# Performance work log

Measured on AMD Instinct MI355X. Metric: run time of the kernel, lower is better.

The kernel has to match this reference:

```python
import jax, jax.numpy as jnp
import numpy as np

N, E, DIN, D, H, L = 4096, 65536, 128, 256, 4, 3
DH = D // H


def _ln(x, g, b, eps=1e-5):
    m = jnp.mean(x, axis=-1, keepdims=True)
    v = jnp.mean((x - m) ** 2, axis=-1, keepdims=True)
    return (x - m) * jax.lax.rsqrt(v + eps) * g + b


def _gcn(x, w, b, row, col, n):
    # PyG GCNConv: add self-loops, symmetric normalization D^-1/2 A D^-1/2, aggregate at col (target)
    ar = jnp.arange(n, dtype=row.dtype)
    r = jnp.concatenate([row, ar])
    c = jnp.concatenate([col, ar])
    deg = jax.ops.segment_sum(jnp.ones(r.shape[0], x.dtype), c, num_segments=n)
    dinv = jnp.where(deg > 0, deg ** -0.5, 0.0)
    norm = dinv[r] * dinv[c]  # (E+N,)
    msg = x @ w.T  # (N, out)
    return jax.ops.segment_sum(norm[:, None] * msg[r], c, num_segments=n) + b


def setup_inputs() -> dict:
    key = jax.random.key(0)
    ks = jax.random.split(key, 12)
    rnd = lambda i, shape: jax.random.normal(ks[i], shape, jnp.float32) * 0.05
    return {
        "node_features": jax.random.normal(ks[0], (N, DIN), jnp.float32),
        "edge_index": jax.random.randint(ks[1], (2, E), 0, N, jnp.int32),
        "gcn1_w": rnd(2, (D, DIN)), "gcn1_b": jnp.zeros((D,), jnp.float32),
        "gcn2_w": rnd(3, (D, D)), "gcn2_b": jnp.zeros((D,), jnp.float32),
        "edge_w": rnd(4, (H, 3)), "edge_b": jnp.zeros((H,), jnp.float32),
        "proj_w": rnd(5, (D, DIN + D)), "proj_b": jnp.zeros((D,), jnp.float32),
        "wqkv": rnd(6, (L, 3 * D, D)), "bqkv": jnp.zeros((L, 3 * D), jnp.float32),
        "wo": rnd(7, (L, D, D)), "bo": jnp.zeros((L, D), jnp.float32),
        "ffn_w1": rnd(8, (L, 4 * D, D)), "ffn_b1": jnp.zeros((L, 4 * D), jnp.float32),
        "ffn_w2": rnd(9, (L, D, 4 * D)), "ffn_b2": jnp.zeros((L, D), jnp.float32),
        "ln1_g": jnp.ones((L, D), jnp.float32), "ln1_b": jnp.zeros((L, D), jnp.float32),
        "ln2_g": jnp.ones((L, D), jnp.float32), "ln2_b": jnp.zeros((L, D), jnp.float32),
        "out_w": rnd(10, (1, D)), "out_b": jnp.zeros((1,), jnp.float32),
    }


def reference(node_features, edge_index, gcn1_w, gcn1_b, gcn2_w, gcn2_b,
              edge_w, edge_b, proj_w, proj_b, wqkv, bqkv, wo, bo,
              ffn_w1, ffn_b1, ffn_w2, ffn_b2, ln1_g, ln1_b, ln2_g, ln2_b,
              out_w, out_b):
    n = node_features.shape[0]
    row, col = edge_index[0], edge_index[1]
    # two-layer GCN
    h = jax.nn.relu(_gcn(node_features, gcn1_w, gcn1_b, row, col, n))
    g = _gcn(h, gcn2_w, gcn2_b, row, col, n)
    x = jnp.concatenate([node_features, g], axis=-1) @ proj_w.T + proj_b  # (N, D)
    # edge-aware attention bias: per-edge linear+sigmoid scattered into dense (H, N, N)
    feat = jnp.stack([row.astype(x.dtype), col.astype(x.dtype),
                      jnp.ones(row.shape[0], x.dtype)], axis=-1)  # (E, 3)
    bpe = jax.nn.sigmoid(feat @ edge_w.T + edge_b)  # (E, H)
    bias = jnp.zeros((H, n, n), x.dtype).at[:, row, col].set(bpe.T)
    scale = 1.0 / np.sqrt(DH)
    for l in range(L):
        qkv = x @ wqkv[l].T + bqkv[l]
        q, k, v = jnp.split(qkv, 3, axis=-1)
        q = q.reshape(n, H, DH); k = k.reshape(n, H, DH); v = v.reshape(n, H, DH)
        s = jnp.einsum('nhd,mhd->hnm', q, k) * scale + bias
        a = jax.nn.softmax(s, axis=-1)
        o = jnp.einsum('hnm,mhd->nhd', a, v).reshape(n, D) @ wo[l].T + bo[l]
        x = _ln(x + o, ln1_g[l], ln1_b[l])
        f = jax.nn.relu(x @ ffn_w1[l].T + ffn_b1[l]) @ ffn_w2[l].T + ffn_b2[l]
        x = _ln(x + f, ln2_g[l], ln2_b[l])
    return jax.nn.sigmoid(x @ out_w.T + out_b)  # (N, 1) probs
```

## Files before the change

kernel.cpp:

```cpp
#include <hip/hip_runtime.h>
#include <math.h>

#define NN 4096
#define NE 65536
#define DIN 128
#define DM 256
#define NH 4
#define NL 3
#define NCH 4
#define TPC (NN / 64 / NCH)
#define NBKT 16384

typedef __attribute__((ext_vector_type(8))) short bf16x8;
typedef __attribute__((ext_vector_type(4))) float f32x4;

__device__ inline ushort f2b(float f) {
    union { float f; uint u; } v; v.f = f;
    uint r = v.u + 0x7fffu + ((v.u >> 16) & 1u);
    return (ushort)(r >> 16);
}

__device__ inline uint cvt_pk_bf16(float lo, float hi) {
    uint r;
    asm("v_cvt_pk_bf16_f32 %0, %1, %2" : "=v"(r) : "v"(lo), "v"(hi));
    return r;
}

__device__ inline void gl_lds16(const ushort* g, ushort* l) {
    __builtin_amdgcn_global_load_lds(
        (const __attribute__((address_space(1))) void*)g,
        (__attribute__((address_space(3))) void*)l, 16, 0, 0);
}


__global__ void k_edge1(const int* __restrict__ row, const int* __restrict__ col,
                        uint* __restrict__ bitmap, int* __restrict__ cnt_c,
                        int* __restrict__ bcnt, unsigned char* __restrict__ flag) {
    int e = blockIdx.x * 256 + threadIdx.x;
    if (e >= NE) return;
    int r = row[e], c = col[e];
    atomicAdd(&cnt_c[c], 1);
    uint idx = (uint)r * 4096u + (uint)c;
    uint m = 1u << (idx & 31);
    uint old = atomicOr(&bitmap[idx >> 5], m);
    int isnew = (old & m) ? 0 : 1;
    flag[e] = (unsigned char)isnew;
    if (isnew) atomicAdd(&bcnt[(r >> 4) * 64 + (c >> 6)], 1);
}

__global__ void k_edge2(const int* __restrict__ row, const int* __restrict__ col,
                        const unsigned char* __restrict__ flag,
                        const int* __restrict__ sc, int* __restrict__ fc, int* __restrict__ csc_row,
                        const int* __restrict__ bstart, int* __restrict__ bfill,
                        uint* __restrict__ entcomb,
                        const float* __restrict__ ew, const float* __restrict__ eb) {
    int e = blockIdx.x * 256 + threadIdx.x;
    if (e >= NE) return;
    int r = row[e], c = col[e];
    csc_row[sc[c] + atomicAdd(&fc[c], 1)] = r;
    if (flag[e]) {
        int key = (r >> 4) * 64 + (c >> 6);
        int pos = bstart[key] + atomicAdd(&bfill[key], 1);
        uint idx = (uint)(((r & 15) << 6) | (c & 63));
        float fr = (float)r, fc2 = (float)c;
#pragma unroll
        for (int h = 0; h < NH; ++h) {
            float arg = ew[h * 3 + 0] * fr + ew[h * 3 + 1] * fc2 + ew[h * 3 + 2] + eb[h];
            float sig = 1.f / (1.f + __expf(-arg));
            entcomb[(long)h * NE + pos] = idx | ((uint)f2b(sig) << 16);
        }
    }
}

template <int N>
__global__ void k_scan(const int* __restrict__ cnt, int* __restrict__ start) {
    __shared__ int part[256];
    const int C = N / 256;
    int t = threadIdx.x;
    int s = 0;
    for (int i = 0; i < C; ++i) s += cnt[t * C + i];
    part[t] = s;
    __syncthreads();
    if (t == 0) {
        int acc = 0;
        for (int i = 0; i < 256; ++i) { int v = part[i]; part[i] = acc; acc += v; }
        start[N] = acc;
    }
    __syncthreads();
    int acc = part[t];
    for (int i = 0; i < C; ++i) { start[t * C + i] = acc; acc += cnt[t * C + i]; }
}

__global__ void k_dinv(const int* __restrict__ cnt_c, float* __restrict__ dinv) {
    int i = blockIdx.x * 256 + threadIdx.x;
    if (i < NN) dinv[i] = 1.0f / sqrtf((float)(cnt_c[i] + 1));
}

struct CvtP { const float* s[8]; ushort* d[8]; int n[8]; };
__global__ void k_cvt(CvtP p) {
    int y = blockIdx.y;
    int base = (blockIdx.x * 256 + threadIdx.x) * 4;
    if (base >= p.n[y]) return;
    float4 v = *(const float4*)(p.s[y] + base);
    float sc = 1.f;
    if (y == 1 && ((base >> 8) % 768) < 256) sc = 0.125f;
    ushort4 o;
    o.x = f2b(v.x * sc); o.y = f2b(v.y * sc); o.z = f2b(v.z * sc); o.w = f2b(v.w * sc);
    *(ushort4*)(p.d[y] + base) = o;
}

__global__ void k_scaleb(const float* __restrict__ b, float* __restrict__ o) {
    int i = blockIdx.x * 256 + threadIdx.x;
    if (i < NL * 768) o[i] = b[i] * (((i % 768) < 256) ? 0.125f : 1.f);
}

template <int FLAGS>
__global__ __launch_bounds__(256) void k_gemm_b(
    const ushort* __restrict__ A, int lda,
    const ushort* __restrict__ B, int ldb,
    float* __restrict__ Cf, ushort* __restrict__ Cb, ushort* __restrict__ Cb2, int ldc,
    int K, const float* __restrict__ bias) {
    __shared__ ushort As[128 * 64];
    __shared__ ushort Bs[128 * 64];
    const int tid = threadIdx.x;
    const int w = tid >> 6, l = tid & 63;
    const int l15 = l & 15, l4 = l >> 4;
    const int row0 = blockIdx.y * 128, col0 = blockIdx.x * 128;
    const int wm = (w >> 1) * 64, wn = (w & 1) * 64;
    f32x4 acc[4][4];
#pragma unroll
    for (int i = 0; i < 4; ++i)
#pragma unroll
        for (int j = 0; j < 4; ++j) acc[i][j] = (f32x4){0.f, 0.f, 0.f, 0.f};
    for (int k0 = 0; k0 < K; k0 += 64) {
#pragma unroll
        for (int i = 0; i < 4; ++i) {
            int ci = tid + 256 * i;
            int r = ci >> 3, s = ci & 7;
            gl_lds16(A + (long)(row0 + r) * lda + k0 + ((s ^ (r & 7)) * 8), &As[ci * 8]);
            gl_lds16(B + (long)(col0 + r) * ldb + k0 + ((s ^ (r & 7)) * 8), &Bs[ci * 8]);
        }
        __syncthreads();
#pragma unroll
        for (int kk = 0; kk < 2; ++kk) {
            bf16x8 af[4], bfr[4];
#pragma unroll
            for (int i = 0; i < 4; ++i) {
                int ar = wm + i * 16 + l15;
                af[i] = *(const bf16x8*)&As[ar * 64 + (((kk * 4 + l4) ^ (ar & 7)) * 8)];
                int br = wn + i * 16 + l15;
                bfr[i] = *(const bf16x8*)&Bs[br * 64 + (((kk * 4 + l4) ^ (br & 7)) * 8)];
            }
#pragma unroll
            for (int i = 0; i < 4; ++i)
#pragma unroll
                for (int j = 0; j < 4; ++j)
                    acc[i][j] = __builtin_amdgcn_mfma_f32_16x16x32_bf16(af[i], bfr[j], acc[i][j], 0, 0, 0);
        }
        __syncthreads();
    }
#pragma unroll
    for (int i = 0; i < 4; ++i)
#pragma unroll
        for (int j = 0; j < 4; ++j) {
            int rb = row0 + wm + i * 16;
            int cb = col0 + wn + j * 16 + l15;
            float bv = bias ? bias[cb] : 0.f;
            if (FLAGS & 16) {
                if (cb < 512) {
#pragma unroll
                    for (int q = 0; q < 4; ++q)
                        Cb[(long)(rb + l4 * 4 + q) * 512 + cb] = f2b(acc[i][j][q] + bv);
                } else {
                    ushort4 o4;
                    o4.x = f2b(acc[i][j][0] + bv);
                    o4.y = f2b(acc[i][j][1] + bv);
                    o4.z = f2b(acc[i][j][2] + bv);
                    o4.w = f2b(acc[i][j][3] + bv);
                    *(ushort4*)(Cb2 + (long)(cb - 512) * NN + rb + l4 * 4) = o4;
                }
            } else if (FLAGS & 8) {
                ushort4 o4;
                o4.x = f2b(acc[i][j][0] + bv);
                o4.y = f2b(acc[i][j][1] + bv);
                o4.z = f2b(acc[i][j][2] + bv);
                o4.w = f2b(acc[i][j][3] + bv);
                *(ushort4*)(Cb + (long)cb * ldc + rb + l4 * 4) = o4;
            } else {
#pragma unroll
                for (int q = 0; q < 4; ++q) {
                    int r = rb + l4 * 4 + q;
                    float v = acc[i][j][q] + bv;
                    if (FLAGS & 4) v = fmaxf(v, 0.f);
                    if (FLAGS & 1) Cf[(long)r * ldc + cb] = v;
                    if (FLAGS & 2) Cb[(long)r * ldc + cb] = f2b(v);
                }
            }
        }
}

__global__ __launch_bounds__(256) void k_gemm_ln(
    const ushort* __restrict__ A, int lda,
    const ushort* __restrict__ B, int ldb, int K,
    const float* __restrict__ bias,
    float* __restrict__ x, ushort* __restrict__ xb,
    const float* __restrict__ gam, const float* __restrict__ bet) {
    __shared__ ushort As[16 * 64];
    __shared__ ushort Bs[256 * 64];
    __shared__ float red[4][16][2];
    const int tid = threadIdx.x;
    const int w = tid >> 6, l = tid & 63;
    const int l15 = l & 15, l4 = l >> 4;
    const int row0 = blockIdx.x * 16;
    f32x4 acc[4];
#pragma unroll
    for (int j = 0; j < 4; ++j) acc[j] = (f32x4){0.f, 0.f, 0.f, 0.f};
    for (int k0 = 0; k0 < K; k0 += 64) {
        if (tid < 128) {
            int r = tid >> 3, s = tid & 7;
            gl_lds16(A + (long)(row0 + r) * lda + k0 + ((s ^ (r & 7)) * 8), &As[tid * 8]);
        }
#pragma unroll
        for (int i = 0; i < 8; ++i) {
            int idx = i * 256 + tid;
            int r = idx >> 3, s = idx & 7;
            gl_lds16(B + (long)r * ldb + k0 + ((s ^ (r & 7)) * 8), &Bs[idx * 8]);
        }
        __syncthreads();
#pragma unroll
        for (int kk = 0; kk < 2; ++kk) {
            bf16x8 af = *(const bf16x8*)&As[l15 * 64 + (((kk * 4 + l4) ^ (l15 & 7)) * 8)];
#pragma unroll
            for (int j = 0; j < 4; ++j) {
                int br = w * 64 + j * 16 + l15;
                bf16x8 bfr = *(const bf16x8*)&Bs[br * 64 + (((kk * 4 + l4) ^ (br & 7)) * 8)];
                acc[j] = __builtin_amdgcn_mfma_f32_16x16x32_bf16(af, bfr, acc[j], 0, 0, 0);
            }
        }
        __syncthreads();
    }
    float val[4][4];
#pragma unroll
    for (int j = 0; j < 4; ++j) {
        int c = w * 64 + j * 16 + l15;
        float bv = bias[c];
#pragma unroll
        for (int q = 0; q < 4; ++q) {
            int r = row0 + l4 * 4 + q;
            val[j][q] = acc[j][q] + bv + x[(long)r * DM + c];
        }
    }
    float sum[4], sq[4];
#pragma unroll
    for (int q = 0; q < 4; ++q) {
        sum[q] = (val[0][q] + val[1][q]) + (val[2][q] + val[3][q]);
        sq[q] = (val[0][q] * val[0][q] + val[1][q] * val[1][q]) +
                (val[2][q] * val[2][q] + val[3][q] * val[3][q]);
    }
#pragma unroll
    for (int o = 1; o < 16; o <<= 1)
#pragma unroll
        for (int q = 0; q < 4; ++q) {
            sum[q] += __shfl_xor(sum[q], o);
            sq[q] += __shfl_xor(sq[q], o);
        }
    if (l15 == 0)
#pragma unroll
        for (int q = 0; q < 4; ++q) {
            red[w][l4 * 4 + q][0] = sum[q];
            red[w][l4 * 4 + q][1] = sq[q];
        }
    __syncthreads();
    float mean[4], rs[4];
#pragma unroll
    for (int q = 0; q < 4; ++q) {
        int rl = l4 * 4 + q;
        float ts = (red[0][rl][0] + red[1][rl][0]) + (red[2][rl][0] + red[3][rl][0]);
        float tq = (red[0][rl][1] + red[1][rl][1]) + (red[2][rl][1] + red[3][rl][1]);
        float m = ts * (1.f / 256.f);
        float var = tq * (1.f / 256.f) - m * m;
        mean[q] = m;
        rs[q] = rsqrtf(var + 1e-5f);
    }
#pragma unroll
    for (int j = 0; j < 4; ++j) {
        int c = w * 64 + j * 16 + l15;
        float gv = gam[c], bv = bet[c];
#pragma unroll
        for (int q = 0; q < 4; ++q) {
            int r = row0 + l4 * 4 + q;
            float ov = (val[j][q] - mean[q]) * rs[q] * gv + bv;
            x[(long)r * DM + c] = ov;
            xb[(long)r * DM + c] = f2b(ov);
        }
    }
}

template <int ACT, int B16>
__global__ void k_gcn_agg(const float* __restrict__ msg, const int* __restrict__ sc,
                          const int* __restrict__ csc_row, const float* __restrict__ dinv,
                          const float* __restrict__ bias,
                          float* __restrict__ outf, ushort* __restrict__ outb) {
    int j = blockIdx.x;
    int d = threadIdx.x;
    float acc = 0.f;
    int a = sc[j], b = sc[j + 1];
    for (int i = a; i < b; ++i) {
        int r = csc_row[i];
        acc += dinv[r] * msg[(long)r * DM + d];
    }
    float dj = dinv[j];
    float v = dj * acc + dj * dj * msg[(long)j * DM + d] + bias[d];
    if (ACT) v = fmaxf(v, 0.f);
    if (B16) outb[(long)j * DM + d] = f2b(v);
    else outf[(long)j * DM + d] = v;
}

__global__ void k_concat(const ushort* __restrict__ nfb, const float* __restrict__ g,
                         ushort* __restrict__ xcb) {
    long i = (long)blockIdx.x * 256 + threadIdx.x;
    if (i >= (long)NN * 384) return;
    int r = (int)(i / 384), c = (int)(i % 384);
    xcb[i] = (c < DIN) ? nfb[(long)r * DIN + c] : f2b(g[(long)r * DM + (c - DIN)]);
}

__global__ __launch_bounds__(256, 4) void k_attn(
    const ushort* __restrict__ qkb, const ushort* __restrict__ vT,
    const int* __restrict__ bstart, const uint* __restrict__ entcomb,
    float* __restrict__ opart, float2* __restrict__ ml) {
    __shared__ ushort Klds[2][4096];
    __shared__ ushort Vlds[2][4096];
    __shared__ ushort Pl[4096];
    const int qb = blockIdx.x, h = blockIdx.y, cz = blockIdx.z;
    const int tid = threadIdx.x, w = tid >> 6, l = tid & 63;
    const int l15 = l & 15, l4 = l >> 4;
    bf16x8 qf[2];
    {
        const ushort* qp = qkb + (long)(qb * 64 + w * 16 + l15) * 512 + h * 64 + l4 * 8;
        qf[0] = *(const bf16x8*)(qp);
        qf[1] = *(const bf16x8*)(qp + 32);
    }
    const ushort* Kb = qkb + 256 + h * 64;
    const ushort* Vb = vT + (long)(h * 64) * NN;
    const uint* ec = entcomb + (long)h * NE;
    f32x4 o[4];
#pragma unroll
    for (int f = 0; f < 4; ++f) o[f] = (f32x4){0.f, 0.f, 0.f, 0.f};
    float m_run = -1e30f, l_run = 0.f;
    char* P = (char*)&Pl[w * 1024];
    const int bktW = (qb * 4 + w) * 64;
    const int t0 = cz * TPC;

    auto stage = [&](int b, int t) {
#pragma unroll
        for (int i = 0; i < 2; ++i) {
            int idx = i * 256 + tid;
            int r = idx >> 3, sl = idx & 7;
            gl_lds16(Kb + (long)(t * 64 + r) * 512 + ((sl ^ (r & 7)) * 8),
                     &Klds[b][idx * 8]);
            gl_lds16(Vb + (long)r * NN + t * 64 + ((sl ^ (r & 7)) * 8),
                     &Vlds[b][idx * 8]);
        }
    };

    int bs_c = bstart[bktW + t0], be_c = bstart[bktW + t0 + 1];
    stage(0, t0);
    int cur = 0;
    for (int tt = 0; tt < TPC; ++tt) {
        const int t = t0 + tt;
        asm volatile("s_waitcnt lgkmcnt(0)" ::: "memory");
        __builtin_amdgcn_s_barrier();
        int bs_n = 0, be_n = 0;
        if (tt + 1 < TPC) {
            stage(cur ^ 1, t + 1);
            bs_n = bstart[bktW + t + 1];
            be_n = bstart[bktW + t + 2];
            asm volatile("s_waitcnt vmcnt(4)" ::: "memory");
        } else {
            asm volatile("s_waitcnt vmcnt(0)" ::: "memory");
        }
        __builtin_amdgcn_sched_barrier(0);
        __builtin_amdgcn_s_barrier();
        __builtin_amdgcn_sched_barrier(0);

        const ushort* Kl = Klds[cur];
        const ushort* Vl = Vlds[cur];
        f32x4 s4[4];
#pragma unroll
        for (int f = 0; f < 4; ++f) {
            int kc = f * 16 + l15;
            bf16x8 k0 = *(const bf16x8*)&Kl[kc * 64 + ((l4 ^ (kc & 7)) * 8)];
            bf16x8 k1 = *(const bf16x8*)&Kl[kc * 64 + (((4 + l4) ^ (kc & 7)) * 8)];
            f32x4 a = (f32x4){0.f, 0.f, 0.f, 0.f};
            a = __builtin_amdgcn_mfma_f32_16x16x32_bf16(k0, qf[0], a, 0, 0, 0);
            a = __builtin_amdgcn_mfma_f32_16x16x32_bf16(k1, qf[1], a, 0, 0, 0);
            s4[f] = a;
        }
        for (int i = bs_c; i < be_c; ++i) {
            uint e = ec[i];
            int r4 = (e >> 6) & 15, c6 = e & 63;
            if (l15 == r4 && ((c6 >> 2) & 3) == l4) {
                union { uint u; float f; } sv;
                sv.u = e & 0xFFFF0000u;
                float sig = sv.f;
                switch (((c6 >> 4) << 2) | (c6 & 3)) {
                    case 0:  s4[0][0] += sig; break; case 1:  s4[0][1] += sig; break;
                    case 2:  s4[0][2] += sig; break; case 3:  s4[0][3] += sig; break;
                    case 4:  s4[1][0] += sig; break; case 5:  s4[1][1] += sig; break;
                    case 6:  s4[1][2] += sig; break; case 7:  s4[1][3] += sig; break;
                    case 8:  s4[2][0] += sig; break; case 9:  s4[2][1] += sig; break;
                    case 10: s4[2][2] += sig; break; case 11: s4[2][3] += sig; break;
                    case 12: s4[3][0] += sig; break; case 13: s4[3][1] += sig; break;
                    case 14: s4[3][2] += sig; break; case 15: s4[3][3] += sig; break;
                }
            }
        }
        float ma = fmaxf(fmaxf(s4[0][0], s4[0][1]), fmaxf(s4[0][2], s4[0][3]));
        float mb = fmaxf(fmaxf(s4[1][0], s4[1][1]), fmaxf(s4[1][2], s4[1][3]));
        float mc = fmaxf(fmaxf(s4[2][0], s4[2][1]), fmaxf(s4[2][2], s4[2][3]));
        float md = fmaxf(fmaxf(s4[3][0], s4[3][1]), fmaxf(s4[3][2], s4[3][3]));
        float me = fmaxf(fmaxf(ma, mb), fmaxf(mc, md));
        me = fmaxf(me, __shfl_xor(me, 16));
        me = fmaxf(me, __shfl_xor(me, 32));
        if (!__all(me <= m_run + 8.f)) {
            float mn = fmaxf(m_run, me);
            float fac = __expf(m_run - mn);
            m_run = mn;
            l_run *= fac;
#pragma unroll
            for (int f = 0; f < 4; ++f)
#pragma unroll
                for (int r = 0; r < 4; ++r) o[f][r] *= fac;
        }
        float rp[4];
#pragma unroll
        for (int f = 0; f < 4; ++f) {
            float p0 = __expf(s4[f][0] - m_run);
            float p1 = __expf(s4[f][1] - m_run);
            float p2 = __expf(s4[f][2] - m_run);
            float p3 = __expf(s4[f][3] - m_run);
            s4[f][0] = p0; s4[f][1] = p1; s4[f][2] = p2; s4[f][3] = p3;
            rp[f] = (p0 + p1) + (p2 + p3);
        }
        float rsum = (rp[0] + rp[1]) + (rp[2] + rp[3]);
        rsum += __shfl_xor(rsum, 16);
        rsum += __shfl_xor(rsum, 32);
        l_run += rsum;
#pragma unroll
        for (int f = 0; f < 4; ++f)
#pragma unroll
            for (int p = 0; p < 2; ++p) {
                uint u = cvt_pk_bf16(s4[f][2 * p], s4[f][2 * p + 1]);
                int slot = f * 2 + (l4 >> 1);
                int byte = l15 * 128 + ((slot ^ (l15 & 7)) << 4) + (l4 & 1) * 8 + p * 4;
                *(uint*)(P + byte) = u;
            }
        asm volatile("s_waitcnt lgkmcnt(0)" ::: "memory");
        __builtin_amdgcn_sched_barrier(0);
#pragma unroll
        for (int ks = 0; ks < 2; ++ks) {
            bf16x8 pb = *(const bf16x8*)(P + l15 * 128 + (((ks * 4 + l4) ^ (l15 & 7)) << 4));
#pragma unroll
            for (int fd = 0; fd < 4; ++fd) {
                int d = fd * 16 + l15;
                bf16x8 vfr = *(const bf16x8*)&Vl[d * 64 + (((ks * 4 + l4) ^ (d & 7)) * 8)];
                o[fd] = __builtin_amdgcn_mfma_f32_16x16x32_bf16(vfr, pb, o[fd], 0, 0, 0);
            }
        }
        bs_c = bs_n; be_c = be_n;
        cur ^= 1;
    }
    long base = (((long)cz * NH + h) * NN + qb * 64 + w * 16 + l15) * 64;
#pragma unroll
    for (int fd = 0; fd < 4; ++fd)
#pragma unroll
        for (int r = 0; r < 4; ++r)
            opart[base + fd * 16 + l4 * 4 + r] = o[fd][r];
    if (l4 == 0)
        ml[((long)cz * NH + h) * NN + qb * 64 + w * 16 + l15] = make_float2(m_run, l_run);
}

__global__ __launch_bounds__(256) void k_comb(const float* __restrict__ opart,
                                              const float2* __restrict__ ml,
                                              ushort* __restrict__ attnOb) {
    int t = blockIdx.x * 256 + threadIdx.x;
    int d = t & 63;
    int r = (t >> 6) & (NN - 1);
    int h = t >> 18;
    float2 mls[NCH];
    float M = -1e30f;
#pragma unroll
    for (int c = 0; c < NCH; ++c) {
        mls[c] = ml[((long)c * NH + h) * NN + r];
        M = fmaxf(M, mls[c].x);
    }
    float s = 0.f, ov = 0.f;
#pragma unroll
    for (int c = 0; c < NCH; ++c) {
        float e = __expf(mls[c].x - M);
        s += mls[c].y * e;
        ov += opart[(((long)c * NH + h) * NN + r) * 64 + d] * e;
    }
    attnOb[(long)r * DM + h * 64 + d] = f2b(ov / s);
}


__global__ void k_out(const float* __restrict__ x, const float* __restrict__ w,
                      const float* __restrict__ b, float* __restrict__ out) {
    int row = blockIdx.x;
    int lane = threadIdx.x;
    float s = 0.f;
#pragma unroll
    for (int i = 0; i < 4; ++i) s += x[(long)row * DM + lane + 64 * i] * w[lane + 64 * i];
#pragma unroll
    for (int o = 1; o < 64; o <<= 1) s += __shfl_xor(s, o);
    if (lane == 0) out[row] = 1.f / (1.f + expf(-(s + b[0])));
}

__global__ void k_sentinel(float* out, int n) {
    int i = blockIdx.x * 256 + threadIdx.x;
    if (i < n) out[i] = 1.0e9f;
}


extern "C" void kernel_launch(void* const* d_in, const int* in_sizes, int n_in,
                              void* d_out, int out_size, void* d_ws, size_t ws_size,
                              hipStream_t stream) {
    const float* nf = (const float*)d_in[0];
    const int* ei = (const int*)d_in[1];
    const int* erow = ei;
    const int* ecol = ei + NE;
    const float* gcn1_w = (const float*)d_in[2];
    const float* gcn1_b = (const float*)d_in[3];
    const float* gcn2_w = (const float*)d_in[4];
    const float* gcn2_b = (const float*)d_in[5];
    const float* edge_w = (const float*)d_in[6];
    const float* edge_b = (const float*)d_in[7];
    const float* proj_w = (const float*)d_in[8];
    const float* proj_b = (const float*)d_in[9];
    const float* wqkv = (const float*)d_in[10];
    const float* bqkv = (const float*)d_in[11];
    const float* wo = (const float*)d_in[12];
    const float* bo = (const float*)d_in[13];
    const float* ffn_w1 = (const float*)d_in[14];
    const float* ffn_b1 = (const float*)d_in[15];
    const float* ffn_w2 = (const float*)d_in[16];
    const float* ffn_b2 = (const float*)d_in[17];
    const float* ln1_g = (const float*)d_in[18];
    const float* ln1_b = (const float*)d_in[19];
    const float* ln2_g = (const float*)d_in[20];
    const float* ln2_b = (const float*)d_in[21];
    const float* out_w = (const float*)d_in[22];
    const float* out_b = (const float*)d_in[23];
    float* out = (float*)d_out;

    char* wp = (char*)d_ws;
    size_t off = 0;
    auto alloc = [&](size_t bytes) -> void* {
        void* p = wp + off;
        off = (off + bytes + 255) & ~(size_t)255;
        return p;
    };
    char* big = (char*)alloc((size_t)NCH * NH * NN * 64 * 4);
    float* msg = (float*)big;
    float* opart = (float*)big;
    ushort* ffnHb = (ushort*)big;
    float* x = (float*)alloc((size_t)NN * DM * 4);
    ushort* xb = (ushort*)alloc((size_t)NN * DM * 2);
    ushort* xcb = (ushort*)alloc((size_t)NN * 384 * 2);
    ushort* hb = (ushort*)alloc((size_t)NN * DM * 2);
    float* g = (float*)alloc((size_t)NN * DM * 4);
    ushort* qkb = (ushort*)alloc((size_t)NN * 512 * 2);
    ushort* vT = (ushort*)alloc((size_t)DM * NN * 2);
    ushort* attnOb = (ushort*)alloc((size_t)NN * DM * 2);
    float2* ml = (float2*)alloc((size_t)NCH * NH * NN * 8);
    ushort* nfb = (ushort*)alloc((size_t)NN * DIN * 2);
    ushort* wqkvb = (ushort*)alloc((size_t)NL * 768 * DM * 2);
    ushort* wob = (ushort*)alloc((size_t)NL * DM * DM * 2);
    ushort* f1b = (ushort*)alloc((size_t)NL * 1024 * DM * 2);
    ushort* f2bw = (ushort*)alloc((size_t)NL * DM * 1024 * 2);
    ushort* g1b = (ushort*)alloc((size_t)DM * DIN * 2);
    ushort* g2b = (ushort*)alloc((size_t)DM * DM * 2);
    ushort* pjb = (ushort*)alloc((size_t)DM * 384 * 2);
    float* bq2 = (float*)alloc((size_t)NL * 768 * 4);
    uint* bitmap = (uint*)alloc((size_t)NN * NN / 8);
    unsigned char* flag = (unsigned char*)alloc(NE);
    int* cnt_c = (int*)alloc((size_t)NN * 4);
    int* bcnt = (int*)alloc((size_t)NBKT * 4);
    int* sc = (int*)alloc((size_t)(NN + 1) * 4);
    int* bstart = (int*)alloc((size_t)(NBKT + 1) * 4);
    int* fc = (int*)alloc((size_t)NN * 4);
    int* bfill = (int*)alloc((size_t)NBKT * 4);
    int* csc_row = (int*)alloc((size_t)NE * 4);
    uint* entcomb = (uint*)alloc((size_t)NH * NE * 4);
    float* dinv = (float*)alloc((size_t)NN * 4);

    if (off > ws_size) {
        k_sentinel<<<(out_size + 255) / 256, 256, 0, stream>>>(out, out_size);
        return;
    }

    hipMemsetAsync(bitmap, 0, (size_t)NN * NN / 8, stream);
    hipMemsetAsync(cnt_c, 0, NN * 4, stream);
    hipMemsetAsync(bcnt, 0, NBKT * 4, stream);
    hipMemsetAsync(fc, 0, NN * 4, stream);
    hipMemsetAsync(bfill, 0, NBKT * 4, stream);
    k_edge1<<<NE / 256, 256, 0, stream>>>(erow, ecol, bitmap, cnt_c, bcnt, flag);
    k_scan<NN><<<1, 256, 0, stream>>>(cnt_c, sc);
    k_scan<NBKT><<<1, 256, 0, stream>>>(bcnt, bstart);
    k_edge2<<<NE / 256, 256, 0, stream>>>(erow, ecol, flag, sc, fc, csc_row, bstart, bfill,
                                          entcomb, edge_w, edge_b);
    k_dinv<<<NN / 256, 256, 0, stream>>>(cnt_c, dinv);

    CvtP cp;
    cp.s[0] = nf;      cp.d[0] = nfb;   cp.n[0] = NN * DIN;
    cp.s[1] = wqkv;    cp.d[1] = wqkvb; cp.n[1] = NL * 768 * DM;
    cp.s[2] = wo;      cp.d[2] = wob;   cp.n[2] = NL * DM * DM;
    cp.s[3] = ffn_w1;  cp.d[3] = f1b;   cp.n[3] = NL * 1024 * DM;
    cp.s[4] = ffn_w2;  cp.d[4] = f2bw;  cp.n[4] = NL * DM * 1024;
    cp.s[5] = gcn1_w;  cp.d[5] = g1b;   cp.n[5] = DM * DIN;
    cp.s[6] = gcn2_w;  cp.d[6] = g2b;   cp.n[6] = DM * DM;
    cp.s[7] = proj_w;  cp.d[7] = pjb;   cp.n[7] = DM * 384;
    k_cvt<<<dim3(768, 8), 256, 0, stream>>>(cp);
    k_scaleb<<<(NL * 768 + 255) / 256, 256, 0, stream>>>(bqkv, bq2);

    k_gemm_b<1><<<dim3(DM / 128, NN / 128), 256, 0, stream>>>(
        nfb, DIN, g1b, DIN, msg, nullptr, nullptr, DM, DIN, nullptr);
    k_gcn_agg<1, 1><<<NN, DM, 0, stream>>>(msg, sc, csc_row, dinv, gcn1_b, nullptr, hb);
    k_gemm_b<1><<<dim3(DM / 128, NN / 128), 256, 0, stream>>>(
        hb, DM, g2b, DM, msg, nullptr, nullptr, DM, DM, nullptr);
    k_gcn_agg<0, 0><<<NN, DM, 0, stream>>>(msg, sc, csc_row, dinv, gcn2_b, g, nullptr);
    k_concat<<<(NN * 384 + 255) / 256, 256, 0, stream>>>(nfb, g, xcb);
    k_gemm_b<3><<<dim3(DM / 128, NN / 128), 256, 0, stream>>>(
        xcb, 384, pjb, 384, x, xb, nullptr, DM, 384, proj_b);

    for (int l = 0; l < NL; ++l) {
        k_gemm_b<18><<<dim3(768 / 128, NN / 128), 256, 0, stream>>>(
            xb, DM, wqkvb + (long)l * 768 * DM, DM, nullptr, qkb, vT, 512, DM,
            bq2 + (long)l * 768);
        k_attn<<<dim3(NN / 64, NH, NCH), 256, 0, stream>>>(
            qkb, vT, bstart, entcomb, opart, ml);
        k_comb<<<NN * NH * 64 / 256, 256, 0, stream>>>(opart, ml, attnOb);
        k_gemm_ln<<<NN / 16, 256, 0, stream>>>(
            attnOb, DM, wob + (long)l * DM * DM, DM, DM, bo + (long)l * DM,
            x, xb, ln1_g + (long)l * DM, ln1_b + (long)l * DM);
        k_gemm_b<6><<<dim3(1024 / 128, NN / 128), 256, 0, stream>>>(
            xb, DM, f1b + (long)l * 1024 * DM, DM, nullptr, ffnHb, nullptr, 1024, DM,
            ffn_b1 + (long)l * 1024);
        k_gemm_ln<<<NN / 16, 256, 0, stream>>>(
            ffnHb, 1024, f2bw + (long)l * DM * 1024, 1024, 1024, ffn_b2 + (long)l * DM,
            x, xb, ln2_g + (long)l * DM, ln2_b + (long)l * DM);
    }
    k_out<<<NN, 64, 0, stream>>>(x, out_w, out_b, out);
}
```

Measured before the change: 478.3 us.

## Fuse concat into projection GEMM and attention combine into out-proj GEMM

Removes the k_concat kernel by having the projection GEMM load node features directly for the first K tiles and convert GCN fp32 output to bf16 on the fly for the rest. Removes k_comb by merging the split-KV attention partials (max/sum rescaling) inside the A-tile load of the output-projection+LayerNorm GEMM. This saves kernel launches and intermediate round trips through global memory. In exchange, A-tile loads become synchronous register loads with conversion instead of async global-to-LDS copies, and the combine work is repeated across column tiles where applicable.

Measured after the change: 464.2 us (median of 2 runs). -2.9%, faster.

```diff
diff --git a/kernel.cpp b/kernel.cpp
--- a/kernel.cpp
+++ b/kernel.cpp
@@ -119,7 +119,7 @@
     const ushort* __restrict__ A, int lda,
     const ushort* __restrict__ B, int ldb,
     float* __restrict__ Cf, ushort* __restrict__ Cb, ushort* __restrict__ Cb2, int ldc,
-    int K, const float* __restrict__ bias) {
+    int K, const float* __restrict__ bias, const float* __restrict__ gsrc) {
     __shared__ ushort As[128 * 64];
     __shared__ ushort Bs[128 * 64];
     const int tid = threadIdx.x;
@@ -137,7 +137,21 @@
         for (int i = 0; i < 4; ++i) {
             int ci = tid + 256 * i;
             int r = ci >> 3, s = ci & 7;
-            gl_lds16(A + (long)(row0 + r) * lda + k0 + ((s ^ (r & 7)) * 8), &As[ci * 8]);
+            if (FLAGS & 32) {
+                if (k0 < 128) {
+                    gl_lds16(A + (long)(row0 + r) * DIN + k0 + ((s ^ (r & 7)) * 8), &As[ci * 8]);
+                } else {
+                    const float* gp = gsrc + (long)(row0 + r) * DM + (k0 - 128) + s * 8;
+                    float4 v0 = *(const float4*)(gp);
+                    float4 v1 = *(const float4*)(gp + 4);
+                    union { bf16x8 v; ushort u[8]; } pk;
+                    pk.u[0] = f2b(v0.x); pk.u[1] = f2b(v0.y); pk.u[2] = f2b(v0.z); pk.u[3] = f2b(v0.w);
+                    pk.u[4] = f2b(v1.x); pk.u[5] = f2b(v1.y); pk.u[6] = f2b(v1.z); pk.u[7] = f2b(v1.w);
+                    *(bf16x8*)&As[r * 64 + ((s ^ (r & 7)) * 8)] = pk.v;
+                }
+            } else {
+                gl_lds16(A + (long)(row0 + r) * lda + k0 + ((s ^ (r & 7)) * 8), &As[ci * 8]);
+            }
             gl_lds16(B + (long)(col0 + r) * ldb + k0 + ((s ^ (r & 7)) * 8), &Bs[ci * 8]);
         }
         __syncthreads();
@@ -199,12 +213,14 @@
         }
 }
 
+template <int COMB>
 __global__ __launch_bounds__(256) void k_gemm_ln(
     const ushort* __restrict__ A, int lda,
     const ushort* __restrict__ B, int ldb, int K,
     const float* __restrict__ bias,
     float* __restrict__ x, ushort* __restrict__ xb,
-    const float* __restrict__ gam, const float* __restrict__ bet) {
+    const float* __restrict__ gam, const float* __restrict__ bet,
+    const float* __restrict__ opart, const float2* __restrict__ ml) {
     __shared__ ushort As[16 * 64];
     __shared__ ushort Bs[256 * 64];
     __shared__ float red[4][16][2];
@@ -218,7 +234,32 @@
     for (int k0 = 0; k0 < K; k0 += 64) {
         if (tid < 128) {
             int r = tid >> 3, s = tid & 7;
-            gl_lds16(A + (long)(row0 + r) * lda + k0 + ((s ^ (r & 7)) * 8), &As[tid * 8]);
+            if (COMB) {
+                int row = row0 + r;
+                int h = k0 >> 6;
+                float2 m0 = ml[(0 * (long)NH + h) * NN + row];
+                float2 m1 = ml[(1 * (long)NH + h) * NN + row];
+                float2 m2 = ml[(2 * (long)NH + h) * NN + row];
+                float2 m3 = ml[(3 * (long)NH + h) * NN + row];
+                float M = fmaxf(fmaxf(m0.x, m1.x), fmaxf(m2.x, m3.x));
+                float e0 = __expf(m0.x - M), e1 = __expf(m1.x - M);
+                float e2 = __expf(m2.x - M), e3 = __expf(m3.x - M);
+                float inv = 1.f / (m0.y * e0 + m1.y * e1 + m2.y * e2 + m3.y * e3);
+                int d0 = s * 8;
+                const float* p0 = opart + ((0 * (long)NH + h) * NN + row) * 64 + d0;
+                const float* p1 = opart + ((1 * (long)NH + h) * NN + row) * 64 + d0;
+                const float* p2 = opart + ((2 * (long)NH + h) * NN + row) * 64 + d0;
+                const float* p3 = opart + ((3 * (long)NH + h) * NN + row) * 64 + d0;
+                union { bf16x8 v; ushort u[8]; } pk;
+#pragma unroll
+                for (int j = 0; j < 8; ++j) {
+                    float ov = e0 * p0[j] + e1 * p1[j] + e2 * p2[j] + e3 * p3[j];
+                    pk.u[j] = f2b(ov * inv);
+                }
+                *(bf16x8*)&As[r * 64 + ((s ^ (r & 7)) * 8)] = pk.v;
+            } else {
+                gl_lds16(A + (long)(row0 + r) * lda + k0 + ((s ^ (r & 7)) * 8), &As[tid * 8]);
+            }
         }
 #pragma unroll
         for (int i = 0; i < 8; ++i) {
@@ -314,14 +355,6 @@
     if (ACT) v = fmaxf(v, 0.f);
     if (B16) outb[(long)j * DM + d] = f2b(v);
     else outf[(long)j * DM + d] = v;
-}
-
-__global__ void k_concat(const ushort* __restrict__ nfb, const float* __restrict__ g,
-                         ushort* __restrict__ xcb) {
-    long i = (long)blockIdx.x * 256 + threadIdx.x;
-    if (i >= (long)NN * 384) return;
-    int r = (int)(i / 384), c = (int)(i % 384);
-    xcb[i] = (c < DIN) ? nfb[(long)r * DIN + c] : f2b(g[(long)r * DM + (c - DIN)]);
 }
 
 __global__ __launch_bounds__(256, 4) void k_attn(
@@ -478,30 +511,6 @@
             opart[base + fd * 16 + l4 * 4 + r] = o[fd][r];
     if (l4 == 0)
         ml[((long)cz * NH + h) * NN + qb * 64 + w * 16 + l15] = make_float2(m_run, l_run);
-}
-
-__global__ __launch_bounds__(256) void k_comb(const float* __restrict__ opart,
-                                              const float2* __restrict__ ml,
-                                              ushort* __restrict__ attnOb) {
-    int t = blockIdx.x * 256 + threadIdx.x;
-    int d = t & 63;
-    int r = (t >> 6) & (NN - 1);
-    int h = t >> 18;
-    float2 mls[NCH];
-    float M = -1e30f;
-#pragma unroll
-    for (int c = 0; c < NCH; ++c) {
-        mls[c] = ml[((long)c * NH + h) * NN + r];
-        M = fmaxf(M, mls[c].x);
-    }
-    float s = 0.f, ov = 0.f;
-#pragma unroll
-    for (int c = 0; c < NCH; ++c) {
-        float e = __expf(mls[c].x - M);
-        s += mls[c].y * e;
-        ov += opart[(((long)c * NH + h) * NN + r) * 64 + d] * e;
-    }
-    attnOb[(long)r * DM + h * 64 + d] = f2b(ov / s);
 }
 
 
@@ -567,12 +576,10 @@
     ushort* ffnHb = (ushort*)big;
     float* x = (float*)alloc((size_t)NN * DM * 4);
     ushort* xb = (ushort*)alloc((size_t)NN * DM * 2);
-    ushort* xcb = (ushort*)alloc((size_t)NN * 384 * 2);
     ushort* hb = (ushort*)alloc((size_t)NN * DM * 2);
     float* g = (float*)alloc((size_t)NN * DM * 4);
     ushort* qkb = (ushort*)alloc((size_t)NN * 512 * 2);
     ushort* vT = (ushort*)alloc((size_t)DM * NN * 2);
-    ushort* attnOb = (ushort*)alloc((size_t)NN * DM * 2);
     float2* ml = (float2*)alloc((size_t)NCH * NH * NN * 8);
     ushort* nfb = (ushort*)alloc((size_t)NN * DIN * 2);
     ushort* wqkvb = (ushort*)alloc((size_t)NL * 768 * DM * 2);
@@ -625,31 +632,29 @@
     k_scaleb<<<(NL * 768 + 255) / 256, 256, 0, stream>>>(bqkv, bq2);
 
     k_gemm_b<1><<<dim3(DM / 128, NN / 128), 256, 0, stream>>>(
-        nfb, DIN, g1b, DIN, msg, nullptr, nullptr, DM, DIN, nullptr);
+        nfb, DIN, g1b, DIN, msg, nullptr, nullptr, DM, DIN, nullptr, nullptr);
     k_gcn_agg<1, 1><<<NN, DM, 0, stream>>>(msg, sc, csc_row, dinv, gcn1_b, nullptr, hb);
     k_gemm_b<1><<<dim3(DM / 128, NN / 128), 256, 0, stream>>>(
-        hb, DM, g2b, DM, msg, nullptr, nullptr, DM, DM, nullptr);
+        hb, DM, g2b, DM, msg, nullptr, nullptr, DM, DM, nullptr, nullptr);
     k_gcn_agg<0, 0><<<NN, DM, 0, stream>>>(msg, sc, csc_row, dinv, gcn2_b, g, nullptr);
-    k_concat<<<(NN * 384 + 255) / 256, 256, 0, stream>>>(nfb, g, xcb);
-    k_gemm_b<3><<<dim3(DM / 128, NN / 128), 256, 0, stream>>>(
-        xcb, 384, pjb, 384, x, xb, nullptr, DM, 384, proj_b);
+    k_gemm_b<35><<<dim3(DM / 128, NN / 128), 256, 0, stream>>>(
+        nfb, DIN, pjb, 384, x, xb, nullptr, DM, 384, proj_b, g);
 
     for (int l = 0; l < NL; ++l) {
         k_gemm_b<18><<<dim3(768 / 128, NN / 128), 256, 0, stream>>>(
             xb, DM, wqkvb + (long)l * 768 * DM, DM, nullptr, qkb, vT, 512, DM,
-            bq2 + (long)l * 768);
+            bq2 + (long)l * 768, nullptr);
         k_attn<<<dim3(NN / 64, NH, NCH), 256, 0, stream>>>(
             qkb, vT, bstart, entcomb, opart, ml);
-        k_comb<<<NN * NH * 64 / 256, 256, 0, stream>>>(opart, ml, attnOb);
-        k_gemm_ln<<<NN / 16, 256, 0, stream>>>(
-            attnOb, DM, wob + (long)l * DM * DM, DM, DM, bo + (long)l * DM,
-            x, xb, ln1_g + (long)l * DM, ln1_b + (long)l * DM);
+        k_gemm_ln<1><<<NN / 16, 256, 0, stream>>>(
+            nullptr, DM, wob + (long)l * DM * DM, DM, DM, bo + (long)l * DM,
+            x, xb, ln1_g + (long)l * DM, ln1_b + (long)l * DM, opart, ml);
         k_gemm_b<6><<<dim3(1024 / 128, NN / 128), 256, 0, stream>>>(
             xb, DM, f1b + (long)l * 1024 * DM, DM, nullptr, ffnHb, nullptr, 1024, DM,
-            ffn_b1 + (long)l * 1024);
-        k_gemm_ln<<<NN / 16, 256, 0, stream>>>(
+            ffn_b1 + (long)l * 1024, nullptr);
+        k_gemm_ln<0><<<NN / 16, 256, 0, stream>>>(
             ffnHb, 1024, f2bw + (long)l * DM * 1024, 1024, 1024, ffn_b2 + (long)l * DM,
-            x, xb, ln2_g + (long)l * DM, ln2_b + (long)l * DM);
+            x, xb, ln2_g + (long)l * DM, ln2_b + (long)l * DM, nullptr, nullptr);
     }
     k_out<<<NN, 64, 0, stream>>>(x, out_w, out_b, out);
 }
```
